# Performance work log

Hardware: AMD Instinct MI355X
Metric: run time of the kernel (lower is better)

Reference implementation:

```python
import jax, jax.numpy as jnp
import numpy as np

N = 50000   # nodes
E = 800000  # edges before self-loops
H = 4       # heads
D = 64      # num_h_feats (per-head out dim of hidden layers)
C = 2       # num_classes
NEG = 0.2   # DGL GATConv leaky_relu negative_slope
EPS = 1e-5  # BatchNorm eps


def setup_inputs() -> dict:
    key = jax.random.key(0)
    ks = jax.random.split(key, 16)
    inp = {}
    inp['feats'] = jax.random.normal(ks[0], (N, 9), jnp.float32)
    inp['W1'] = jax.random.normal(ks[1], (9, H * D), jnp.float32) * 0.1
    inp['al1'] = jax.random.normal(ks[2], (H, D), jnp.float32) * 0.1
    inp['ar1'] = jax.random.normal(ks[3], (H, D), jnp.float32) * 0.1
    inp['b1'] = jnp.zeros((H, D), jnp.float32)
    inp['Wm'] = jax.random.normal(ks[4], (D, H * D), jnp.float32) * 0.1
    inp['alm'] = jax.random.normal(ks[5], (H, D), jnp.float32) * 0.1
    inp['arm'] = jax.random.normal(ks[6], (H, D), jnp.float32) * 0.1
    inp['bm'] = jnp.zeros((H, D), jnp.float32)
    inp['W2'] = jax.random.normal(ks[7], (D, H * C), jnp.float32) * 0.1
    inp['al2'] = jax.random.normal(ks[8], (H, C), jnp.float32) * 0.1
    inp['ar2'] = jax.random.normal(ks[9], (H, C), jnp.float32) * 0.1
    inp['b2'] = jnp.zeros((H, C), jnp.float32)
    inp['gamma'] = jnp.ones((D,), jnp.float32)
    inp['beta'] = jnp.zeros((D,), jnp.float32)
    inp['src'] = jax.random.randint(ks[10], (E,), 0, N, jnp.int32)
    inp['dst'] = jax.random.randint(ks[11], (E,), 0, N, jnp.int32)
    return inp


def gat_layer(x, W, al, ar, b, src, dst, out_d):
    """DGL GATConv: linear -> per-edge attention -> dst-softmax -> scatter-sum."""
    n = x.shape[0]
    z = (x @ W).reshape(n, H, out_d)                 # [N, H, Dout]
    el = jnp.sum(z * al, axis=-1)                    # [N, H] attn on src
    er = jnp.sum(z * ar, axis=-1)                    # [N, H] attn on dst
    e = jax.nn.leaky_relu(el[src] + er[dst], NEG)    # [E, H]
    m = jax.ops.segment_max(e, dst, num_segments=n)  # per-dst max (stable softmax)
    a = jnp.exp(e - m[dst])
    s = jax.ops.segment_sum(a, dst, num_segments=n)
    alpha = a / s[dst]                               # [E, H]
    out = jax.ops.segment_sum(alpha[:, :, None] * z[src], dst, num_segments=n)
    return out + b                                   # [N, H, Dout]


def batchnorm(h, gamma, beta):
    mu = jnp.mean(h, axis=0)
    var = jnp.var(h, axis=0)
    return (h - mu) * jax.lax.rsqrt(var + EPS) * gamma + beta


def reference(feats, W1, al1, ar1, b1, Wm, alm, arm, bm, W2, al2, ar2, b2,
              gamma, beta, src, dst):
    # dgl.add_self_loop
    loop = jnp.arange(N, dtype=src.dtype)
    s = jnp.concatenate([src, loop])
    d = jnp.concatenate([dst, loop])
    h = gat_layer(feats, W1, al1, ar1, b1, s, d, D).sum(axis=1)  # head-sum
    h = batchnorm(h, gamma, beta)
    h = gat_layer(h, Wm, alm, arm, bm, s, d, D).sum(axis=1)
    h = batchnorm(h, gamma, beta)
    o = gat_layer(h, W2, al2, ar2, b2, s, d, C).sum(axis=1)      # [N, C]
    return o
```

## Files before the change

kernel.cpp:

```cpp
#include <hip/hip_runtime.h>
#include <hip/hip_bf16.h>

typedef __hip_bfloat16 bf16;
typedef __bf16 bf16x8 __attribute__((ext_vector_type(8)));
typedef float f32x4 __attribute__((ext_vector_type(4)));
typedef _Float16 h16;
typedef _Float16 h16x4 __attribute__((ext_vector_type(4)));

__device__ __forceinline__ float b2f(bf16 v) { return __bfloat162float(v); }

__device__ __forceinline__ float ldin(const void* p, size_t i, int isb) {
    return isb ? b2f(((const bf16*)p)[i]) : ((const float*)p)[i];
}
__device__ __forceinline__ unsigned short f2bfbits(float f) {
    bf16 v = __float2bfloat16(f);
    return *(unsigned short*)&v;
}

__global__ __launch_bounds__(256) void prep_kernel(
    const void* __restrict__ feats, const void* __restrict__ W1, const void* __restrict__ Wm,
    const void* __restrict__ al1, const void* __restrict__ ar1,
    const void* __restrict__ alm, const void* __restrict__ arm,
    const unsigned* __restrict__ gbits,
    unsigned short* __restrict__ fpad, unsigned short* __restrict__ W1T,
    unsigned short* __restrict__ WmT,
    float* __restrict__ alf1, float* __restrict__ arf1,
    float* __restrict__ alfm, float* __restrict__ arfm,
    int* __restrict__ flag, int Nn) {
    int isb = (gbits[0] == 0x3F803F80u) ? 1 : 0;
    long t = (long)blockIdx.x * 256 + threadIdx.x;
    if (t == 0) *flag = isb;
    long n64 = (long)Nn * 64;
    if (t < n64) {
        int k = (int)(t & 63); long n = t >> 6;
        fpad[t] = (k < 9) ? f2bfbits(ldin(feats, (size_t)n * 9 + k, isb)) : 0;
    } else if (t < n64 + 16384) {
        long u = t - n64; int n = (int)(u >> 6), k = (int)(u & 63);
        W1T[u] = (k < 9) ? f2bfbits(ldin(W1, (size_t)k * 256 + n, isb)) : 0;
    } else if (t < n64 + 32768) {
        long u = t - n64 - 16384; int n = (int)(u >> 6), k = (int)(u & 63);
        WmT[u] = f2bfbits(ldin(Wm, (size_t)k * 256 + n, isb));
    } else if (t < n64 + 32768 + 256) {
        int u = (int)(t - n64 - 32768);
        alf1[u] = ldin(al1, u, isb); arf1[u] = ldin(ar1, u, isb);
        alfm[u] = ldin(alm, u, isb); arfm[u] = ldin(arm, u, isb);
    }
}

__global__ __launch_bounds__(256) void count_kernel(
    const int* __restrict__ dst, int* __restrict__ deg, int E) {
    int t = blockIdx.x * 256 + threadIdx.x;
    if (t < E) atomicAdd(&deg[dst[t]], 1);
}

__global__ __launch_bounds__(256) void scan1_kernel(
    const int* __restrict__ deg, int* __restrict__ off, int* __restrict__ bsum, int Nn) {
    __shared__ int s[256];
    int t = threadIdx.x, i = blockIdx.x * 256 + t;
    int v = (i < Nn) ? deg[i] : 0;
    s[t] = v; __syncthreads();
#pragma unroll
    for (int o = 1; o < 256; o <<= 1) {
        int a = (t >= o) ? s[t - o] : 0;
        __syncthreads();
        s[t] += a;
        __syncthreads();
    }
    if (i < Nn) off[i] = s[t];
    if (t == 255) bsum[blockIdx.x] = s[255];
}

__global__ __launch_bounds__(256) void scan2_kernel(int* __restrict__ bsum, int NB) {
    __shared__ int s[256];
    int t = threadIdx.x;
    int v = (t < NB) ? bsum[t] : 0;
    s[t] = v; __syncthreads();
#pragma unroll
    for (int o = 1; o < 256; o <<= 1) {
        int a = (t >= o) ? s[t - o] : 0;
        __syncthreads();
        s[t] += a;
        __syncthreads();
    }
    if (t < NB) bsum[t] = s[t] - v;
}

__global__ __launch_bounds__(256) void scan3_kernel(
    const int* __restrict__ deg, int* __restrict__ off, int* __restrict__ cur,
    const int* __restrict__ bsum, int Nn, int E) {
    int i = blockIdx.x * 256 + threadIdx.x;
    if (i < Nn) {
        int ex = off[i] - deg[i] + bsum[i >> 8];
        off[i] = ex;
        cur[i] = ex;
    }
    if (i == 0) off[Nn] = E;
}

__global__ __launch_bounds__(256) void scatter_kernel(
    const int* __restrict__ src, const int* __restrict__ dst,
    int* __restrict__ cur, int* __restrict__ adj, int E) {
    int t = blockIdx.x * 256 + threadIdx.x;
    if (t < E) {
        int p = atomicAdd(&cur[dst[t]], 1);
        adj[p] = src[t];
    }
}

__global__ __launch_bounds__(256) void lin_mfma_kernel(
    const unsigned short* __restrict__ xb, const unsigned short* __restrict__ WT,
    const float* __restrict__ alf, const float* __restrict__ arf,
    h16* __restrict__ zh, float* __restrict__ el, float* __restrict__ er, int Nn) {
    int w = threadIdx.x >> 6;
    int l = threadIdx.x & 63;
    int quad = l >> 4, lc = l & 15;
    int node0 = blockIdx.x * 16;

    int mrow = node0 + lc; if (mrow >= Nn) mrow = Nn - 1;
    const bf16x8* xa = (const bf16x8*)(xb + (size_t)mrow * 64);
    bf16x8 a0 = xa[quad];
    bf16x8 a1 = xa[quad + 4];

    float pe[4] = {0.f, 0.f, 0.f, 0.f}, pr[4] = {0.f, 0.f, 0.f, 0.f};
    int row0 = node0 + quad * 4;
#pragma unroll
    for (int ct = 0; ct < 4; ++ct) {
        int col = w * 64 + ct * 16 + lc;
        const bf16x8* wb = (const bf16x8*)(WT + (size_t)col * 64);
        bf16x8 b0 = wb[quad];
        bf16x8 b1 = wb[quad + 4];
        f32x4 c = {0.f, 0.f, 0.f, 0.f};
        c = __builtin_amdgcn_mfma_f32_16x16x32_bf16(a0, b0, c, 0, 0, 0);
        c = __builtin_amdgcn_mfma_f32_16x16x32_bf16(a1, b1, c, 0, 0, 0);
        float av = alf[col], rv = arf[col];
#pragma unroll
        for (int r = 0; r < 4; ++r) {
            pe[r] = fmaf(c[r], av, pe[r]);
            pr[r] = fmaf(c[r], rv, pr[r]);
            int n = row0 + r;
            if (n < Nn) zh[(size_t)n * 256 + col] = (h16)c[r];
        }
    }
#pragma unroll
    for (int o = 1; o < 16; o <<= 1) {
#pragma unroll
        for (int r = 0; r < 4; ++r) {
            pe[r] += __shfl_xor(pe[r], o);
            pr[r] += __shfl_xor(pr[r], o);
        }
    }
    if (lc == 0) {
#pragma unroll
        for (int r = 0; r < 4; ++r) {
            int n = row0 + r;
            if (n < Nn) { el[n * 4 + w] = pe[r]; er[n * 4 + w] = pr[r]; }
        }
    }
}

__global__ __launch_bounds__(256) void lin3_kernel(
    const unsigned short* __restrict__ xb,
    const void* __restrict__ W, const void* __restrict__ al, const void* __restrict__ ar,
    float* __restrict__ zc, float* __restrict__ el, float* __restrict__ er,
    const int* __restrict__ flag, int Nn) {
    int isb = *flag;
    int t = blockIdx.x * 256 + threadIdx.x;
    if (t >= Nn * 4) return;
    int n = t >> 2, h = t & 3;
    const bf16* xr = (const bf16*)(xb + (size_t)n * 64);
    float a0 = 0.f, a1 = 0.f;
#pragma unroll 8
    for (int k = 0; k < 64; k++) {
        float xv = b2f(xr[k]);
        a0 += xv * ldin(W, k * 8 + h * 2 + 0, isb);
        a1 += xv * ldin(W, k * 8 + h * 2 + 1, isb);
    }
    zc[n * 8 + h * 2 + 0] = a0;
    zc[n * 8 + h * 2 + 1] = a1;
    el[t] = a0 * ldin(al, h * 2, isb) + a1 * ldin(al, h * 2 + 1, isb);
    er[t] = a0 * ldin(ar, h * 2, isb) + a1 * ldin(ar, h * 2 + 1, isb);
}

__global__ __launch_bounds__(256) void gat_agg64_kernel(
    const h16* __restrict__ zh, const float* __restrict__ el, const float* __restrict__ er,
    const int* __restrict__ off, const int* __restrict__ adj, const void* __restrict__ bias,
    float* __restrict__ x, float* __restrict__ bnsum, float* __restrict__ bnsumsq,
    const int* __restrict__ flag, int Nn, int total_waves) {
    __shared__ __align__(16) float s_sum[4][64], s_sq[4][64];
    int isb = *flag;
    int tid = threadIdx.x;
    int wv = tid >> 6;
    int l = tid & 63;
    int h = l >> 4, q = l & 15;
    int gw = blockIdx.x * 4 + wv;

    float4 bsl;
    bsl.x = ldin(bias, h * 64 + q * 4 + 0, isb);
    bsl.y = ldin(bias, h * 64 + q * 4 + 1, isb);
    bsl.z = ldin(bias, h * 64 + q * 4 + 2, isb);
    bsl.w = ldin(bias, h * 64 + q * 4 + 3, isb);

    float4 bs = {0.f, 0.f, 0.f, 0.f}, bq = {0.f, 0.f, 0.f, 0.f};

    for (int n = gw; n < Nn; n += total_waves) {
        float er_nh = er[n * 4 + h];
        float e0 = el[n * 4 + h] + er_nh;
        e0 = (e0 > 0.f) ? e0 : 0.2f * e0;
        float w0 = __expf(e0);
        h16x4 zsh = ((const h16x4*)(zh + (size_t)n * 256))[h * 16 + q];
        float4 acc;
        acc.x = w0 * (float)zsh.x; acc.y = w0 * (float)zsh.y;
        acc.z = w0 * (float)zsh.z; acc.w = w0 * (float)zsh.w;
        float lsum = w0;
        int s0 = off[n], s1 = off[n + 1];
        for (int i = s0; i < s1; i += 8) {
            int ss[8];
#pragma unroll
            for (int j = 0; j < 8; j++) {
                int idx = i + j;
                ss[j] = adj[idx < s1 ? idx : s1 - 1];
            }
            float ev[8];
#pragma unroll
            for (int j = 0; j < 8; j++) ev[j] = el[ss[j] * 4 + h];
            h16x4 zv[8];
#pragma unroll
            for (int j = 0; j < 8; j++)
                zv[j] = ((const h16x4*)(zh + (size_t)ss[j] * 256))[h * 16 + q];
#pragma unroll
            for (int j = 0; j < 8; j++) {
                float e = ev[j] + er_nh;
                e = (e > 0.f) ? e : 0.2f * e;
                float w = __expf(e);
                if (i + j >= s1) w = 0.f;
                lsum += w;
                acc.x = fmaf(w, (float)zv[j].x, acc.x);
                acc.y = fmaf(w, (float)zv[j].y, acc.y);
                acc.z = fmaf(w, (float)zv[j].z, acc.z);
                acc.w = fmaf(w, (float)zv[j].w, acc.w);
            }
        }
        float inv = 1.f / lsum;
        float4 r;
        r.x = fmaf(acc.x, inv, bsl.x);
        r.y = fmaf(acc.y, inv, bsl.y);
        r.z = fmaf(acc.z, inv, bsl.z);
        r.w = fmaf(acc.w, inv, bsl.w);
#pragma unroll
        for (int o = 16; o < 64; o <<= 1) {
            r.x += __shfl_xor(r.x, o);
            r.y += __shfl_xor(r.y, o);
            r.z += __shfl_xor(r.z, o);
            r.w += __shfl_xor(r.w, o);
        }
        if (h == 0) {
            ((float4*)(x + (size_t)n * 64))[q] = r;
            bs.x += r.x; bs.y += r.y; bs.z += r.z; bs.w += r.w;
            bq.x = fmaf(r.x, r.x, bq.x); bq.y = fmaf(r.y, r.y, bq.y);
            bq.z = fmaf(r.z, r.z, bq.z); bq.w = fmaf(r.w, r.w, bq.w);
        }
    }
    if (h == 0) {
        ((float4*)&s_sum[wv][0])[q] = bs;
        ((float4*)&s_sq[wv][0])[q] = bq;
    }
    __syncthreads();
    if (tid < 64) {
        float s = s_sum[0][tid] + s_sum[1][tid] + s_sum[2][tid] + s_sum[3][tid];
        float qq = s_sq[0][tid] + s_sq[1][tid] + s_sq[2][tid] + s_sq[3][tid];
        atomicAdd(&bnsum[tid], s);
        atomicAdd(&bnsumsq[tid], qq);
    }
}

__global__ __launch_bounds__(256) void bn_apply_kernel(
    const float* __restrict__ x, const float* __restrict__ bnsum, const float* __restrict__ bnsumsq,
    const void* __restrict__ gamma, const void* __restrict__ beta,
    unsigned short* __restrict__ xb, const int* __restrict__ flag, int Nn) {
    int isb = *flag;
    int t = blockIdx.x * 256 + threadIdx.x;
    if (t >= Nn * 64) return;
    int d = t & 63;
    float inv_n = 1.f / (float)Nn;
    float mu = bnsum[d] * inv_n;
    float var = bnsumsq[d] * inv_n - mu * mu;
    float s = rsqrtf(var + 1e-5f) * ldin(gamma, d, isb);
    float sh = ldin(beta, d, isb) - mu * s;
    xb[t] = f2bfbits(fmaf(x[t], s, sh));
}

__global__ __launch_bounds__(256) void gat_agg2_kernel(
    const float* __restrict__ zc, const float* __restrict__ el, const float* __restrict__ er,
    const int* __restrict__ off, const int* __restrict__ adj, const void* __restrict__ bias,
    void* __restrict__ out, const int* __restrict__ flag, int Nn) {
    int isb = *flag;
    int n = blockIdx.x * 256 + threadIdx.x;
    if (n >= Nn) return;
    float4 eln = ((const float4*)el)[n];
    float4 ern = ((const float4*)er)[n];
    float4 z0 = ((const float4*)zc)[n * 2];
    float4 z1 = ((const float4*)zc)[n * 2 + 1];
    float w[4], lh[4];
    {
        float ev[4] = {eln.x + ern.x, eln.y + ern.y, eln.z + ern.z, eln.w + ern.w};
#pragma unroll
        for (int hh = 0; hh < 4; hh++) {
            float e = ev[hh];
            e = (e > 0.f) ? e : 0.2f * e;
            w[hh] = __expf(e);
            lh[hh] = w[hh];
        }
    }
    float4 a0, a1;
    a0.x = w[0] * z0.x; a0.y = w[0] * z0.y; a0.z = w[1] * z0.z; a0.w = w[1] * z0.w;
    a1.x = w[2] * z1.x; a1.y = w[2] * z1.y; a1.z = w[3] * z1.z; a1.w = w[3] * z1.w;
    int s0 = off[n], s1 = off[n + 1];
    for (int i = s0; i < s1; i += 4) {
        int ss[4];
#pragma unroll
        for (int j = 0; j < 4; j++) {
            int idx = i + j; if (idx >= s1) idx = s1 - 1;
            ss[j] = adj[idx];
        }
        float4 elj[4], zj0[4], zj1[4];
#pragma unroll
        for (int j = 0; j < 4; j++) {
            elj[j] = ((const float4*)el)[ss[j]];
            zj0[j] = ((const float4*)zc)[ss[j] * 2];
            zj1[j] = ((const float4*)zc)[ss[j] * 2 + 1];
        }
#pragma unroll
        for (int j = 0; j < 4; j++) {
            if (i + j < s1) {
                float ev[4] = {elj[j].x + ern.x, elj[j].y + ern.y, elj[j].z + ern.z, elj[j].w + ern.w};
                float wj[4];
#pragma unroll
                for (int hh = 0; hh < 4; hh++) {
                    float e = ev[hh];
                    e = (e > 0.f) ? e : 0.2f * e;
                    wj[hh] = __expf(e);
                    lh[hh] += wj[hh];
                }
                a0.x = fmaf(wj[0], zj0[j].x, a0.x); a0.y = fmaf(wj[0], zj0[j].y, a0.y);
                a0.z = fmaf(wj[1], zj0[j].z, a0.z); a0.w = fmaf(wj[1], zj0[j].w, a0.w);
                a1.x = fmaf(wj[2], zj1[j].x, a1.x); a1.y = fmaf(wj[2], zj1[j].y, a1.y);
                a1.z = fmaf(wj[3], zj1[j].z, a1.z); a1.w = fmaf(wj[3], zj1[j].w, a1.w);
            }
        }
    }
    float v0 = a0.x / lh[0] + a0.z / lh[1] + a1.x / lh[2] + a1.z / lh[3]
             + ldin(bias, 0, isb) + ldin(bias, 2, isb) + ldin(bias, 4, isb) + ldin(bias, 6, isb);
    float v1 = a0.y / lh[0] + a0.w / lh[1] + a1.y / lh[2] + a1.w / lh[3]
             + ldin(bias, 1, isb) + ldin(bias, 3, isb) + ldin(bias, 5, isb) + ldin(bias, 7, isb);
    if (isb) {
        ((bf16*)out)[n * 2 + 0] = __float2bfloat16(v0);
        ((bf16*)out)[n * 2 + 1] = __float2bfloat16(v1);
    } else {
        ((float*)out)[n * 2 + 0] = v0;
        ((float*)out)[n * 2 + 1] = v1;
    }
}

extern "C" void kernel_launch(void* const* d_in, const int* in_sizes, int n_in,
                              void* d_out, int out_size, void* d_ws, size_t ws_size,
                              hipStream_t stream) {
    const void* feats = d_in[0];
    const void* W1    = d_in[1];
    const void* al1   = d_in[2];
    const void* ar1   = d_in[3];
    const void* b1    = d_in[4];
    const void* Wm    = d_in[5];
    const void* alm   = d_in[6];
    const void* arm   = d_in[7];
    const void* bm    = d_in[8];
    const void* W2    = d_in[9];
    const void* al2   = d_in[10];
    const void* ar2   = d_in[11];
    const void* b2v   = d_in[12];
    const void* gamma = d_in[13];
    const void* beta  = d_in[14];
    const int*  src   = (const int*)d_in[15];
    const int*  dst   = (const int*)d_in[16];

    int Nn = in_sizes[0] / 9;
    int E  = in_sizes[15];

    float* ws = (float*)d_ws;
    h16*   zh   = (h16*)ws;
    float* zc   = ws + (size_t)Nn * 128;
    float* el   = zc + (size_t)Nn * 8;
    float* er   = el + (size_t)Nn * 4;
    float* x    = er + (size_t)Nn * 4;
    float* bns  = x + (size_t)Nn * 64;
    float* bnq  = bns + 64;
    float* alf1 = bnq + 64;
    float* arf1 = alf1 + 256;
    float* alfm = arf1 + 256;
    float* arfm = alfm + 256;
    unsigned short* xb   = (unsigned short*)(arfm + 256);
    unsigned short* fpad = xb + (size_t)Nn * 64;
    unsigned short* W1T  = fpad + (size_t)Nn * 64;
    unsigned short* WmT  = W1T + 256 * 64;
    int*   flag = (int*)(WmT + 256 * 64);
    int*   deg  = flag + 1;
    int*   off  = deg + Nn;
    int*   cur  = off + Nn + 1;
    int*   adj  = cur + Nn;
    int*   bsum = adj + E;

    dim3 B(256);
    int NB1 = (Nn + 255) / 256;
    int gE  = (E + 255) / 256;
    int gN64 = (Nn * 64 + 255) / 256;
    int gMF  = (Nn + 15) / 16;
    long prepN = (long)Nn * 64 + 32768 + 256;
    int gPrep = (int)((prepN + 255) / 256);
    int AGG_GRID = 2048;
    int total_waves = AGG_GRID * 4;

    prep_kernel<<<gPrep, B, 0, stream>>>(feats, W1, Wm, al1, ar1, alm, arm,
                                         (const unsigned*)gamma, fpad, W1T, WmT,
                                         alf1, arf1, alfm, arfm, flag, Nn);

    hipMemsetAsync(deg, 0, (size_t)Nn * sizeof(int), stream);
    count_kernel<<<gE, B, 0, stream>>>(dst, deg, E);
    scan1_kernel<<<NB1, B, 0, stream>>>(deg, off, bsum, Nn);
    scan2_kernel<<<1, B, 0, stream>>>(bsum, NB1);
    scan3_kernel<<<NB1, B, 0, stream>>>(deg, off, cur, bsum, Nn, E);
    scatter_kernel<<<gE, B, 0, stream>>>(src, dst, cur, adj, E);

    hipMemsetAsync(bns, 0, 128 * sizeof(float), stream);
    lin_mfma_kernel<<<gMF, B, 0, stream>>>(fpad, W1T, alf1, arf1, zh, el, er, Nn);
    gat_agg64_kernel<<<AGG_GRID, B, 0, stream>>>(zh, el, er, off, adj, b1, x, bns, bnq, flag, Nn, total_waves);
    bn_apply_kernel<<<gN64, B, 0, stream>>>(x, bns, bnq, gamma, beta, xb, flag, Nn);

    hipMemsetAsync(bns, 0, 128 * sizeof(float), stream);
    lin_mfma_kernel<<<gMF, B, 0, stream>>>(xb, WmT, alfm, arfm, zh, el, er, Nn);
    gat_agg64_kernel<<<AGG_GRID, B, 0, stream>>>(zh, el, er, off, adj, bm, x, bns, bnq, flag, Nn, total_waves);
    bn_apply_kernel<<<gN64, B, 0, stream>>>(x, bns, bnq, gamma, beta, xb, flag, Nn);

    lin3_kernel<<<(Nn * 4 + 255) / 256, B, 0, stream>>>(xb, W2, al2, ar2, zc, el, er, flag, Nn);
    gat_agg2_kernel<<<NB1, B, 0, stream>>>(zc, el, er, off, adj, b2v, d_out, flag, Nn);
}
```

Before: 474.8 us.

## Fuse batchnorm apply into next linear, stage MFMA output in LDS, split agg2 per head

The elementwise bn_apply passes are replaced by a tiny coefficient kernel, and the normalization is folded into the following MFMA linear kernel and lin3. This removes a full read and write of the N×64 activation twice. The MFMA kernels now stage their fp16 outputs in shared memory and write them out with coalesced 16-byte stores instead of scattered 2-byte stores. The final aggregation kernel uses one thread per (node, head) with a shuffle reduction, raising parallelism at the cost of more redundant adjacency reads. The BN memsets are also merged into one up front.

```diff
diff --git a/kernel.cpp b/kernel.cpp
--- a/kernel.cpp
+++ b/kernel.cpp
@@ -107,10 +107,12 @@
     }
 }
 
-__global__ __launch_bounds__(256) void lin_mfma_kernel(
+
+__global__ __launch_bounds__(256) void lin_mfma_l1_kernel(
     const unsigned short* __restrict__ xb, const unsigned short* __restrict__ WT,
     const float* __restrict__ alf, const float* __restrict__ arf,
     h16* __restrict__ zh, float* __restrict__ el, float* __restrict__ er, int Nn) {
+    __shared__ h16 zs[16 * 256];
     int w = threadIdx.x >> 6;
     int l = threadIdx.x & 63;
     int quad = l >> 4, lc = l & 15;
@@ -122,7 +124,7 @@
     bf16x8 a1 = xa[quad + 4];
 
     float pe[4] = {0.f, 0.f, 0.f, 0.f}, pr[4] = {0.f, 0.f, 0.f, 0.f};
-    int row0 = node0 + quad * 4;
+    int row0 = quad * 4;
 #pragma unroll
     for (int ct = 0; ct < 4; ++ct) {
         int col = w * 64 + ct * 16 + lc;
@@ -137,8 +139,7 @@
         for (int r = 0; r < 4; ++r) {
             pe[r] = fmaf(c[r], av, pe[r]);
             pr[r] = fmaf(c[r], rv, pr[r]);
-            int n = row0 + r;
-            if (n < Nn) zh[(size_t)n * 256 + col] = (h16)c[r];
+            zs[(row0 + r) * 256 + col] = (h16)c[r];
         }
     }
 #pragma unroll
@@ -152,14 +153,127 @@
     if (lc == 0) {
 #pragma unroll
         for (int r = 0; r < 4; ++r) {
-            int n = row0 + r;
+            int n = node0 + row0 + r;
             if (n < Nn) { el[n * 4 + w] = pe[r]; er[n * 4 + w] = pr[r]; }
         }
     }
+    __syncthreads();
+#pragma unroll
+    for (int it = 0; it < 2; ++it) {
+        int flat = it * 2048 + threadIdx.x * 8;
+        int row = flat >> 8;
+        if (node0 + row < Nn)
+            *(uint4*)(zh + (size_t)node0 * 256 + flat) = *(const uint4*)(zs + flat);
+    }
+}
+
+__global__ __launch_bounds__(256) void lin_mfma_bn_kernel(
+    const float* __restrict__ x, const float* __restrict__ sc, const float* __restrict__ shb,
+    const unsigned short* __restrict__ WT,
+    const float* __restrict__ alf, const float* __restrict__ arf,
+    h16* __restrict__ zh, float* __restrict__ el, float* __restrict__ er, int Nn) {
+    __shared__ h16 zs[16 * 256];
+    int w = threadIdx.x >> 6;
+    int l = threadIdx.x & 63;
+    int quad = l >> 4, lc = l & 15;
+    int node0 = blockIdx.x * 16;
+
+    int mrow = node0 + lc; if (mrow >= Nn) mrow = Nn - 1;
+    const float* xr = x + (size_t)mrow * 64 + quad * 8;
+    float4 f0 = ((const float4*)xr)[0];
+    float4 f1 = ((const float4*)xr)[1];
+    float4 f2 = ((const float4*)(xr + 32))[0];
+    float4 f3 = ((const float4*)(xr + 32))[1];
+    float4 s0 = ((const float4*)(sc + quad * 8))[0];
+    float4 s1 = ((const float4*)(sc + quad * 8))[1];
+    float4 s2 = ((const float4*)(sc + 32 + quad * 8))[0];
+    float4 s3 = ((const float4*)(sc + 32 + quad * 8))[1];
+    float4 h0 = ((const float4*)(shb + quad * 8))[0];
+    float4 h1 = ((const float4*)(shb + quad * 8))[1];
+    float4 h2 = ((const float4*)(shb + 32 + quad * 8))[0];
+    float4 h3 = ((const float4*)(shb + 32 + quad * 8))[1];
+
+    union { bf16x8 v; unsigned short s[8]; } ua, ub;
+    ua.s[0] = f2bfbits(fmaf(f0.x, s0.x, h0.x));
+    ua.s[1] = f2bfbits(fmaf(f0.y, s0.y, h0.y));
+    ua.s[2] = f2bfbits(fmaf(f0.z, s0.z, h0.z));
+    ua.s[3] = f2bfbits(fmaf(f0.w, s0.w, h0.w));
+    ua.s[4] = f2bfbits(fmaf(f1.x, s1.x, h1.x));
+    ua.s[5] = f2bfbits(fmaf(f1.y, s1.y, h1.y));
+    ua.s[6] = f2bfbits(fmaf(f1.z, s1.z, h1.z));
+    ua.s[7] = f2bfbits(fmaf(f1.w, s1.w, h1.w));
+    ub.s[0] = f2bfbits(fmaf(f2.x, s2.x, h2.x));
+    ub.s[1] = f2bfbits(fmaf(f2.y, s2.y, h2.y));
+    ub.s[2] = f2bfbits(fmaf(f2.z, s2.z, h2.z));
+    ub.s[3] = f2bfbits(fmaf(f2.w, s2.w, h2.w));
+    ub.s[4] = f2bfbits(fmaf(f3.x, s3.x, h3.x));
+    ub.s[5] = f2bfbits(fmaf(f3.y, s3.y, h3.y));
+    ub.s[6] = f2bfbits(fmaf(f3.z, s3.z, h3.z));
+    ub.s[7] = f2bfbits(fmaf(f3.w, s3.w, h3.w));
+    bf16x8 a0 = ua.v, a1 = ub.v;
+
+    float pe[4] = {0.f, 0.f, 0.f, 0.f}, pr[4] = {0.f, 0.f, 0.f, 0.f};
+    int row0 = quad * 4;
+#pragma unroll
+    for (int ct = 0; ct < 4; ++ct) {
+        int col = w * 64 + ct * 16 + lc;
+        const bf16x8* wb = (const bf16x8*)(WT + (size_t)col * 64);
+        bf16x8 b0 = wb[quad];
+        bf16x8 b1 = wb[quad + 4];
+        f32x4 c = {0.f, 0.f, 0.f, 0.f};
+        c = __builtin_amdgcn_mfma_f32_16x16x32_bf16(a0, b0, c, 0, 0, 0);
+        c = __builtin_amdgcn_mfma_f32_16x16x32_bf16(a1, b1, c, 0, 0, 0);
+        float av = alf[col], rv = arf[col];
+#pragma unroll
+        for (int r = 0; r < 4; ++r) {
+            pe[r] = fmaf(c[r], av, pe[r]);
+            pr[r] = fmaf(c[r], rv, pr[r]);
+            zs[(row0 + r) * 256 + col] = (h16)c[r];
+        }
+    }
+#pragma unroll
+    for (int o = 1; o < 16; o <<= 1) {
+#pragma unroll
+        for (int r = 0; r < 4; ++r) {
+            pe[r] += __shfl_xor(pe[r], o);
+            pr[r] += __shfl_xor(pr[r], o);
+        }
+    }
+    if (lc == 0) {
+#pragma unroll
+        for (int r = 0; r < 4; ++r) {
+            int n = node0 + row0 + r;
+            if (n < Nn) { el[n * 4 + w] = pe[r]; er[n * 4 + w] = pr[r]; }
+        }
+    }
+    __syncthreads();
+#pragma unroll
+    for (int it = 0; it < 2; ++it) {
+        int flat = it * 2048 + threadIdx.x * 8;
+        int row = flat >> 8;
+        if (node0 + row < Nn)
+            *(uint4*)(zh + (size_t)node0 * 256 + flat) = *(const uint4*)(zs + flat);
+    }
+}
+
+__global__ void bn_coef_kernel(
+    const float* __restrict__ bnsum, const float* __restrict__ bnsumsq,
+    const void* __restrict__ gamma, const void* __restrict__ beta,
+    float* __restrict__ sc, float* __restrict__ shb,
+    const int* __restrict__ flag, int Nn) {
+    int isb = *flag;
+    int d = threadIdx.x;
+    if (d >= 64) return;
+    float inv_n = 1.f / (float)Nn;
+    float mu = bnsum[d] * inv_n;
+    float var = bnsumsq[d] * inv_n - mu * mu;
+    float s = rsqrtf(var + 1e-5f) * ldin(gamma, d, isb);
+    sc[d] = s;
+    shb[d] = ldin(beta, d, isb) - mu * s;
 }
 
 __global__ __launch_bounds__(256) void lin3_kernel(
-    const unsigned short* __restrict__ xb,
+    const float* __restrict__ x, const float* __restrict__ sc, const float* __restrict__ shb,
     const void* __restrict__ W, const void* __restrict__ al, const void* __restrict__ ar,
     float* __restrict__ zc, float* __restrict__ el, float* __restrict__ er,
     const int* __restrict__ flag, int Nn) {
@@ -167,13 +281,13 @@
     int t = blockIdx.x * 256 + threadIdx.x;
     if (t >= Nn * 4) return;
     int n = t >> 2, h = t & 3;
-    const bf16* xr = (const bf16*)(xb + (size_t)n * 64);
+    const float* xr = x + (size_t)n * 64;
     float a0 = 0.f, a1 = 0.f;
 #pragma unroll 8
     for (int k = 0; k < 64; k++) {
-        float xv = b2f(xr[k]);
-        a0 += xv * ldin(W, k * 8 + h * 2 + 0, isb);
-        a1 += xv * ldin(W, k * 8 + h * 2 + 1, isb);
+        float xn = fmaf(xr[k], sc[k], shb[k]);
+        a0 += xn * ldin(W, k * 8 + h * 2 + 0, isb);
+        a1 += xn * ldin(W, k * 8 + h * 2 + 1, isb);
     }
     zc[n * 8 + h * 2 + 0] = a0;
     zc[n * 8 + h * 2 + 1] = a1;
@@ -273,47 +387,21 @@
     }
 }
 
-__global__ __launch_bounds__(256) void bn_apply_kernel(
-    const float* __restrict__ x, const float* __restrict__ bnsum, const float* __restrict__ bnsumsq,
-    const void* __restrict__ gamma, const void* __restrict__ beta,
-    unsigned short* __restrict__ xb, const int* __restrict__ flag, int Nn) {
-    int isb = *flag;
-    int t = blockIdx.x * 256 + threadIdx.x;
-    if (t >= Nn * 64) return;
-    int d = t & 63;
-    float inv_n = 1.f / (float)Nn;
-    float mu = bnsum[d] * inv_n;
-    float var = bnsumsq[d] * inv_n - mu * mu;
-    float s = rsqrtf(var + 1e-5f) * ldin(gamma, d, isb);
-    float sh = ldin(beta, d, isb) - mu * s;
-    xb[t] = f2bfbits(fmaf(x[t], s, sh));
-}
-
 __global__ __launch_bounds__(256) void gat_agg2_kernel(
     const float* __restrict__ zc, const float* __restrict__ el, const float* __restrict__ er,
     const int* __restrict__ off, const int* __restrict__ adj, const void* __restrict__ bias,
     void* __restrict__ out, const int* __restrict__ flag, int Nn) {
     int isb = *flag;
-    int n = blockIdx.x * 256 + threadIdx.x;
-    if (n >= Nn) return;
-    float4 eln = ((const float4*)el)[n];
-    float4 ern = ((const float4*)er)[n];
-    float4 z0 = ((const float4*)zc)[n * 2];
-    float4 z1 = ((const float4*)zc)[n * 2 + 1];
-    float w[4], lh[4];
-    {
-        float ev[4] = {eln.x + ern.x, eln.y + ern.y, eln.z + ern.z, eln.w + ern.w};
-#pragma unroll
-        for (int hh = 0; hh < 4; hh++) {
-            float e = ev[hh];
-            e = (e > 0.f) ? e : 0.2f * e;
-            w[hh] = __expf(e);
-            lh[hh] = w[hh];
-        }
-    }
-    float4 a0, a1;
-    a0.x = w[0] * z0.x; a0.y = w[0] * z0.y; a0.z = w[1] * z0.z; a0.w = w[1] * z0.w;
-    a1.x = w[2] * z1.x; a1.y = w[2] * z1.y; a1.z = w[3] * z1.z; a1.w = w[3] * z1.w;
+    int t = blockIdx.x * 256 + threadIdx.x;
+    if (t >= Nn * 4) return;
+    int n = t >> 2, h = t & 3;
+    float er_nh = er[n * 4 + h];
+    float e0 = el[n * 4 + h] + er_nh;
+    e0 = (e0 > 0.f) ? e0 : 0.2f * e0;
+    float w0 = __expf(e0);
+    float lsum = w0;
+    float2 zn = ((const float2*)zc)[n * 4 + h];
+    float a0 = w0 * zn.x, a1 = w0 * zn.y;
     int s0 = off[n], s1 = off[n + 1];
     for (int i = s0; i < s1; i += 4) {
         int ss[4];
@@ -322,42 +410,39 @@
             int idx = i + j; if (idx >= s1) idx = s1 - 1;
             ss[j] = adj[idx];
         }
-        float4 elj[4], zj0[4], zj1[4];
+        float ev[4]; float2 zj[4];
 #pragma unroll
         for (int j = 0; j < 4; j++) {
-            elj[j] = ((const float4*)el)[ss[j]];
-            zj0[j] = ((const float4*)zc)[ss[j] * 2];
-            zj1[j] = ((const float4*)zc)[ss[j] * 2 + 1];
+            ev[j] = el[ss[j] * 4 + h];
+            zj[j] = ((const float2*)zc)[ss[j] * 4 + h];
         }
 #pragma unroll
         for (int j = 0; j < 4; j++) {
-            if (i + j < s1) {
-                float ev[4] = {elj[j].x + ern.x, elj[j].y + ern.y, elj[j].z + ern.z, elj[j].w + ern.w};
-                float wj[4];
-#pragma unroll
-                for (int hh = 0; hh < 4; hh++) {
-                    float e = ev[hh];
-                    e = (e > 0.f) ? e : 0.2f * e;
-                    wj[hh] = __expf(e);
-                    lh[hh] += wj[hh];
-                }
-                a0.x = fmaf(wj[0], zj0[j].x, a0.x); a0.y = fmaf(wj[0], zj0[j].y, a0.y);
-                a0.z = fmaf(wj[1], zj0[j].z, a0.z); a0.w = fmaf(wj[1], zj0[j].w, a0.w);
-                a1.x = fmaf(wj[2], zj1[j].x, a1.x); a1.y = fmaf(wj[2], zj1[j].y, a1.y);
-                a1.z = fmaf(wj[3], zj1[j].z, a1.z); a1.w = fmaf(wj[3], zj1[j].w, a1.w);
-            }
-        }
-    }
-    float v0 = a0.x / lh[0] + a0.z / lh[1] + a1.x / lh[2] + a1.z / lh[3]
-             + ldin(bias, 0, isb) + ldin(bias, 2, isb) + ldin(bias, 4, isb) + ldin(bias, 6, isb);
-    float v1 = a0.y / lh[0] + a0.w / lh[1] + a1.y / lh[2] + a1.w / lh[3]
-             + ldin(bias, 1, isb) + ldin(bias, 3, isb) + ldin(bias, 5, isb) + ldin(bias, 7, isb);
-    if (isb) {
-        ((bf16*)out)[n * 2 + 0] = __float2bfloat16(v0);
-        ((bf16*)out)[n * 2 + 1] = __float2bfloat16(v1);
-    } else {
-        ((float*)out)[n * 2 + 0] = v0;
-        ((float*)out)[n * 2 + 1] = v1;
+            float e = ev[j] + er_nh;
+            e = (e > 0.f) ? e : 0.2f * e;
+            float w = __expf(e);
+            if (i + j >= s1) w = 0.f;
+            lsum += w;
+            a0 = fmaf(w, zj[j].x, a0);
+            a1 = fmaf(w, zj[j].y, a1);
+        }
+    }
+    float inv = 1.f / lsum;
+    float v0 = fmaf(a0, inv, ldin(bias, h * 2 + 0, isb));
+    float v1 = fmaf(a1, inv, ldin(bias, h * 2 + 1, isb));
+#pragma unroll
+    for (int o = 1; o < 4; o <<= 1) {
+        v0 += __shfl_xor(v0, o);
+        v1 += __shfl_xor(v1, o);
+    }
+    if (h == 0) {
+        if (isb) {
+            ((bf16*)out)[n * 2 + 0] = __float2bfloat16(v0);
+            ((bf16*)out)[n * 2 + 1] = __float2bfloat16(v1);
+        } else {
+            ((float*)out)[n * 2 + 0] = v0;
+            ((float*)out)[n * 2 + 1] = v1;
+        }
     }
 }
 
@@ -391,14 +476,19 @@
     float* el   = zc + (size_t)Nn * 8;
     float* er   = el + (size_t)Nn * 4;
     float* x    = er + (size_t)Nn * 4;
-    float* bns  = x + (size_t)Nn * 64;
-    float* bnq  = bns + 64;
-    float* alf1 = bnq + 64;
+    float* bns1 = x + (size_t)Nn * 64;
+    float* bnq1 = bns1 + 64;
+    float* bns2 = bnq1 + 64;
+    float* bnq2 = bns2 + 64;
+    float* sc1  = bnq2 + 64;
+    float* shb1 = sc1 + 64;
+    float* sc2  = shb1 + 64;
+    float* shb2 = sc2 + 64;
+    float* alf1 = shb2 + 64;
     float* arf1 = alf1 + 256;
     float* alfm = arf1 + 256;
     float* arfm = alfm + 256;
-    unsigned short* xb   = (unsigned short*)(arfm + 256);
-    unsigned short* fpad = xb + (size_t)Nn * 64;
+    unsigned short* fpad = (unsigned short*)(arfm + 256);
     unsigned short* W1T  = fpad + (size_t)Nn * 64;
     unsigned short* WmT  = W1T + 256 * 64;
     int*   flag = (int*)(WmT + 256 * 64);
@@ -411,8 +501,8 @@
     dim3 B(256);
     int NB1 = (Nn + 255) / 256;
     int gE  = (E + 255) / 256;
-    int gN64 = (Nn * 64 + 255) / 256;
     int gMF  = (Nn + 15) / 16;
+    int gN4 = (Nn * 4 + 255) / 256;
     long prepN = (long)Nn * 64 + 32768 + 256;
     int gPrep = (int)((prepN + 255) / 256);
     int AGG_GRID = 2048;
@@ -423,22 +513,21 @@
                                          alf1, arf1, alfm, arfm, flag, Nn);
 
     hipMemsetAsync(deg, 0, (size_t)Nn * sizeof(int), stream);
+    hipMemsetAsync(bns1, 0, 256 * sizeof(float), stream);
     count_kernel<<<gE, B, 0, stream>>>(dst, deg, E);
     scan1_kernel<<<NB1, B, 0, stream>>>(deg, off, bsum, Nn);
     scan2_kernel<<<1, B, 0, stream>>>(bsum, NB1);
     scan3_kernel<<<NB1, B, 0, stream>>>(deg, off, cur, bsum, Nn, E);
     scatter_kernel<<<gE, B, 0, stream>>>(src, dst, cur, adj, E);
 
-    hipMemsetAsync(bns, 0, 128 * sizeof(float), stream);
-    lin_mfma_kernel<<<gMF, B, 0, stream>>>(fpad, W1T, alf1, arf1, zh, el, er, Nn);
-    gat_agg64_kernel<<<AGG_GRID, B, 0, stream>>>(zh, el, er, off, adj, b1, x, bns, bnq, flag, Nn, total_waves);
-    bn_apply_kernel<<<gN64, B, 0, stream>>>(x, bns, bnq, gamma, beta, xb, flag, Nn);
-
-    hipMemsetAsync(bns, 0, 128 * sizeof(float), stream);
-    lin_mfma_kernel<<<gMF, B, 0, stream>>>(xb, WmT, alfm, arfm, zh, el, er, Nn);
-    gat_agg64_kernel<<<AGG_GRID, B, 0, stream>>>(zh, el, er, off, adj, bm, x, bns, bnq, flag, Nn, total_waves);
-    bn_apply_kernel<<<gN64, B, 0, stream>>>(x, bns, bnq, gamma, beta, xb, flag, Nn);
-
-    lin3_kernel<<<(Nn * 4 + 255) / 256, B, 0, stream>>>(xb, W2, al2, ar2, zc, el, er, flag, Nn);
-    gat_agg2_kernel<<<NB1, B, 0, stream>>>(zc, el, er, off, adj, b2v, d_out, flag, Nn);
-}
+    lin_mfma_l1_kernel<<<gMF, B, 0, stream>>>(fpad, W1T, alf1, arf1, zh, el, er, Nn);
+    gat_agg64_kernel<<<AGG_GRID, B, 0, stream>>>(zh, el, er, off, adj, b1, x, bns1, bnq1, flag, Nn, total_waves);
+    bn_coef_kernel<<<1, 64, 0, stream>>>(bns1, bnq1, gamma, beta, sc1, shb1, flag, Nn);
+
+    lin_mfma_bn_kernel<<<gMF, B, 0, stream>>>(x, sc1, shb1, WmT, alfm, arfm, zh, el, er, Nn);
+    gat_agg64_kernel<<<AGG_GRID, B, 0, stream>>>(zh, el, er, off, adj, bm, x, bns2, bnq2, flag, Nn, total_waves);
+    bn_coef_kernel<<<1, 64, 0, stream>>>(bns2, bnq2, gamma, beta, sc2, shb2, flag, Nn);
+
+    lin3_kernel<<<gN4, B, 0, stream>>>(x, sc2, shb2, W2, al2, ar2, zc, el, er, flag, Nn);
+    gat_agg2_kernel<<<gN4, B, 0, stream>>>(zc, el, er, off, adj, b2v, d_out, flag, Nn);
+}
```

Result: no change. 468.6 us (-1.3%).
